# Performance work log

Hardware: AMD Instinct MI355X
Metric: run time of the kernel (lower is better)

The kernel has to match this reference:

```python
import jax, jax.numpy as jnp
import numpy as np

NUM_HEADS = 8
WIN = (7, 7)


def _relative_position_index(wh, ww):
    # Same construction as the torch module (numpy, static).
    coords = np.stack(np.meshgrid(np.arange(wh), np.arange(ww), indexing='ij'))  # (2, wh, ww)
    flat = coords.reshape(2, -1)                                                 # (2, L)
    rel = flat[:, :, None] - flat[:, None, :]                                    # (2, L, L)
    rel = rel.transpose(1, 2, 0).astype(np.int64)                                # (L, L, 2)
    rel[:, :, 0] += wh - 1
    rel[:, :, 1] += ww - 1
    rel[:, :, 0] *= 2 * ww - 1
    return rel.sum(-1)  # (L, L), values in [0, (2wh-1)*(2ww-1))


def setup_inputs() -> dict:
    key = jax.random.key(0)
    k0, k1, k2, k3, k4 = jax.random.split(key, 5)
    B, C = 2048, 256
    wh, ww = WIN
    L = wh * ww
    nW = 64
    q = jax.random.normal(k0, (B, C, wh, ww), dtype=jnp.float32)
    k = jax.random.normal(k1, (B, C, wh, ww), dtype=jnp.float32)
    v = jax.random.normal(k2, (B, C, wh, ww), dtype=jnp.float32)
    # Swin-style shift mask: 0 where attend, -100 where blocked
    keep = jax.random.uniform(k3, (nW, L, L)) < 0.9
    mask = jnp.where(keep, 0.0, -100.0).astype(jnp.float32)
    n_bias = (2 * wh - 1) * (2 * ww - 1)  # 169
    rel_bias_table = 0.02 * jax.random.normal(k4, (n_bias, NUM_HEADS), dtype=jnp.float32)
    rel_pos_index = jnp.asarray(_relative_position_index(wh, ww), dtype=jnp.int32)
    return {"q": q, "k": k, "v": v, "mask": mask,
            "rel_bias_table": rel_bias_table, "rel_pos_index": rel_pos_index}


def reference(q, k, v, mask, rel_bias_table, rel_pos_index):
    b, c, wh, ww = q.shape
    L = wh * ww
    H = NUM_HEADS
    d_k = c // H
    scale = d_k ** -0.5
    qh = q.reshape(b, H, d_k, L)
    kh = k.reshape(b, H, d_k, L)
    # NOTE: the original torch code reassigns v = k.reshape(...) — values come from k.
    vh = kh
    attn = jnp.einsum('bhct,bhcs->bhts', qh, kh) * scale  # (b, H, L, L)
    bias = rel_bias_table[rel_pos_index.reshape(-1)].reshape(L, L, H)
    attn = attn + jnp.transpose(bias, (2, 0, 1))[None]    # (1, H, L, L)
    nW = mask.shape[0]
    attn = attn.reshape(b // nW, nW, H, L, L) + mask[None, :, None]
    attn = attn.reshape(b, H, L, L)
    attn = jax.nn.softmax(attn, axis=-1)
    score = jnp.einsum('bhts,bhcs->bhct', attn, vh).reshape(b, c, wh, ww)
    return (score, attn)
```

## Files before the change

kernel.cpp:

```cpp
#include <hip/hip_runtime.h>
#include <hip/hip_bf16.h>
#include <math.h>


#define LW 49
#define NH 8

typedef short s16x8 __attribute__((ext_vector_type(8)));
typedef float f32x4 __attribute__((ext_vector_type(4)));
typedef unsigned short u16x4 __attribute__((ext_vector_type(4)));

union Frag { s16x8 v; unsigned short u[8]; };

__device__ __forceinline__ unsigned short f2bf(float x) {
    return __builtin_bit_cast(unsigned short, __float2bfloat16(x));
}
__device__ __forceinline__ float bf2f(unsigned short h) {
    return __uint_as_float(((unsigned)h) << 16);
}
__device__ __forceinline__ void split8(const float* xf, Frag& hi, Frag& lo) {
    #pragma unroll
    for (int j = 0; j < 8; j++) {
        const unsigned short hb = f2bf(xf[j]);
        hi.u[j] = hb;
        lo.u[j] = f2bf(xf[j] - bf2f(hb));
    }
}

__device__ __forceinline__ void lds_barrier() {
    asm volatile("s_waitcnt lgkmcnt(0)" ::: "memory");
    __builtin_amdgcn_s_barrier();
    asm volatile("" ::: "memory");
    __builtin_amdgcn_sched_barrier(0);
}

#define MFMA16(A, B, C) __builtin_amdgcn_mfma_f32_16x16x32_bf16((A), (B), (C), 0, 0, 0)

__global__ __launch_bounds__(256) void prep_frag_kernel(
    const float* __restrict__ mask, const float* __restrict__ table,
    const int* __restrict__ idx,
    unsigned short* __restrict__ biasB, unsigned short* __restrict__ maskB)
{
    const int i = blockIdx.x * 256 + threadIdx.x;
    const int NBF = 8 * 4096;
    const int NMF = 64 * 4096;
    const float L2E = 1.4426950408889634f;
    if (i < NBF) {
        const int h = i >> 12, rem = i & 4095;
        const int gi = rem >> 8, lane = (rem >> 2) & 63, r = rem & 3;
        const int mt = gi >> 2, nt = gi & 3;
        const int t = mt * 16 + (lane >> 4) * 4 + r;
        const int s = nt * 16 + (lane & 15);
        const float v = (t < LW && s < LW)
                      ? table[idx[t * LW + s] * NH + h] * L2E : 0.f;
        biasB[i] = f2bf(v);
    } else if (i < NBF + NMF) {
        const int j = i - NBF;
        const int w2 = j >> 12, rem = j & 4095;
        const int gi = rem >> 8, lane = (rem >> 2) & 63, r = rem & 3;
        const int mt = gi >> 2, nt = gi & 3;
        const int t = mt * 16 + (lane >> 4) * 4 + r;
        const int s = nt * 16 + (lane & 15);
        const float v = (t < LW && s < LW)
                      ? mask[w2 * (LW * LW) + t * LW + s] * L2E : 0.f;
        maskB[j] = f2bf(v);
    }
}

__global__ __launch_bounds__(128, 4) void wa_mfma_kernel(
    const float* __restrict__ q, const float* __restrict__ k,
    const unsigned short* __restrict__ biasB,
    const unsigned short* __restrict__ maskB,
    float* __restrict__ score_out, float* __restrict__ attn_out)
{
    __shared__ __align__(16) unsigned short sB[6272];

    const int wv   = __builtin_amdgcn_readfirstlane((int)(threadIdx.x >> 6));
    const int bh   = blockIdx.x;
    const int h    = bh & 7;
    const int w    = (bh >> 3) & 63;
    const int lane = threadIdx.x & 63;
    const int l15  = lane & 15;
    const int g4   = lane >> 4;

    const float* qp = q + (size_t)bh * (32 * LW);
    const float* kp = k + (size_t)bh * (32 * LW);

    float k1raw[2][8], qraw[2][8], k2raw[2][8];
    #pragma unroll
    for (int ki = 0; ki < 2; ki++) {
        const int s  = (wv * 2 + ki) * 16 + l15;
        const int sc = s < LW ? s : (LW - 1);
        #pragma unroll
        for (int j = 0; j < 8; j++) k1raw[ki][j] = kp[(g4 * 8 + j) * LW + sc];
    }
    #pragma unroll
    for (int mi = 0; mi < 2; mi++) {
        const int t  = (wv * 2 + mi) * 16 + l15;
        const int tc = t < LW ? t : (LW - 1);
        #pragma unroll
        for (int j = 0; j < 8; j++) qraw[mi][j] = qp[(g4 * 8 + j) * LW + tc];
    }
    {
        const int c = wv * 16 + l15;
        #pragma unroll
        for (int ks = 0; ks < 2; ks++)
            #pragma unroll
            for (int j = 0; j < 8; j++) {
                const int s  = ks * 32 + g4 * 8 + j;
                const int sc = s < LW ? s : (LW - 1);
                k2raw[ks][j] = kp[c * LW + sc];
            }
    }

    u16x4 bq4[2][4], mq4[2][4];
    {
        const unsigned short* bF = biasB + (size_t)h * 4096 + lane * 4;
        const unsigned short* mF = maskB + (size_t)w * 4096 + lane * 4;
        #pragma unroll
        for (int mi = 0; mi < 2; mi++)
            #pragma unroll
            for (int nt = 0; nt < 4; nt++) {
                const int gi = (wv * 2 + mi) * 4 + nt;
                bq4[mi][nt] = *(const u16x4*)(bF + gi * 256);
                mq4[mi][nt] = *(const u16x4*)(mF + gi * 256);
            }
    }

    #pragma unroll
    for (int ki = 0; ki < 2; ki++) {
        const int nt = wv * 2 + ki;
        Frag Kh, Kl;
        split8(k1raw[ki], Kh, Kl);
        *(s16x8*)&sB[nt * 512 + lane * 8]        = Kh.v;
        *(s16x8*)&sB[2048 + nt * 512 + lane * 8] = Kl.v;
    }

    Frag Qh[2], Ql[2];
    split8(qraw[0], Qh[0], Ql[0]);
    split8(qraw[1], Qh[1], Ql[1]);

    lds_barrier();

    f32x4 acc[2][4];
    #pragma unroll
    for (int mi = 0; mi < 2; mi++)
        #pragma unroll
        for (int nt = 0; nt < 4; nt++)
            #pragma unroll
            for (int r = 0; r < 4; r++) acc[mi][nt][r] = 0.f;

    #pragma unroll
    for (int nt = 0; nt < 4; nt++) {
        Frag Kh, Kl;
        Kh.v = *(const s16x8*)&sB[nt * 512 + lane * 8];
        Kl.v = *(const s16x8*)&sB[2048 + nt * 512 + lane * 8];
        #pragma unroll
        for (int mi = 0; mi < 2; mi++) {
            acc[mi][nt] = MFMA16(Qh[mi].v, Kh.v, acc[mi][nt]);
            acc[mi][nt] = MFMA16(Ql[mi].v, Kh.v, acc[mi][nt]);
            acc[mi][nt] = MFMA16(Qh[mi].v, Kl.v, acc[mi][nt]);
        }
    }

    const float scale2 = 0.17677669529663687f * 1.4426950408889634f;
    #pragma unroll
    for (int mi = 0; mi < 2; mi++) {
        #pragma unroll
        for (int nt = 0; nt < 4; nt++) {
            const bool pad = (nt * 16 + l15) >= LW;
            #pragma unroll
            for (int r = 0; r < 4; r++) {
                const float bm = bf2f(bq4[mi][nt][r]) + bf2f(mq4[mi][nt][r]);
                const float v2 = fmaf(acc[mi][nt][r], scale2, bm);
                acc[mi][nt][r] = pad ? -1e30f : v2;
            }
        }
    }

    #pragma unroll
    for (int mi = 0; mi < 2; mi++) {
        #pragma unroll
        for (int r = 0; r < 4; r++) {
            float sm = 0.f;
            #pragma unroll
            for (int nt = 0; nt < 4; nt++) {
                const float p = __builtin_exp2f(acc[mi][nt][r]);
                acc[mi][nt][r] = p;
                sm += p;
            }
            sm += __shfl_xor(sm, 1);
            sm += __shfl_xor(sm, 2);
            sm += __shfl_xor(sm, 4);
            sm += __shfl_xor(sm, 8);
            const float inv = 1.0f / sm;
            #pragma unroll
            for (int nt = 0; nt < 4; nt++) acc[mi][nt][r] *= inv;
        }
    }

    lds_barrier();

    #pragma unroll
    for (int mi = 0; mi < 2; mi++) {
        #pragma unroll
        for (int r = 0; r < 4; r++) {
            const int t = (wv * 2 + mi) * 16 + g4 * 4 + r;
            if (t < LW) {
                #pragma unroll
                for (int nt = 0; nt < 4; nt++) {
                    const int s = nt * 16 + l15;
                    const float p = acc[mi][nt][r];
                    const unsigned short ph = f2bf(p);
                    const unsigned short pl = f2bf(p - bf2f(ph));
                    const unsigned idx = (unsigned)t * 64u
                        + ((((unsigned)s >> 3) ^ ((unsigned)t & 7u)) << 3)
                        + ((unsigned)s & 7u);
                    sB[idx]        = ph;
                    sB[3136 + idx] = pl;
                }
            }
        }
    }

    lds_barrier();

    float* attn_base = attn_out + (size_t)bh * (LW * LW);
    #pragma unroll
    for (int mi = 0; mi < 2; mi++) {
        #pragma unroll
        for (int r = 0; r < 4; r++) {
            const int t = (wv * 2 + mi) * 16 + g4 * 4 + r;
            if (t < LW) {
                #pragma unroll
                for (int nt = 0; nt < 4; nt++) {
                    const int s = nt * 16 + l15;
                    if (s < LW) attn_base[t * LW + s] = acc[mi][nt][r];
                }
            }
        }
    }

    Frag K2h[2], K2l[2];
    split8(k2raw[0], K2h[0], K2l[0]);
    split8(k2raw[1], K2h[1], K2l[1]);

    f32x4 acc2[4];
    #pragma unroll
    for (int nt = 0; nt < 4; nt++)
        #pragma unroll
        for (int r = 0; r < 4; r++) acc2[nt][r] = 0.f;

    #pragma unroll
    for (int ntt = 0; ntt < 4; ntt++) {
        const int t  = ntt * 16 + l15;
        const int tr = t < LW ? t : (LW - 1);
        #pragma unroll
        for (int ks = 0; ks < 2; ks++) {
            const unsigned base = (unsigned)tr * 64u
                + (((unsigned)(ks * 4 + g4) ^ ((unsigned)tr & 7u)) << 3);
            Frag Ph, Pl;
            Ph.v = *(const s16x8*)&sB[base];
            Pl.v = *(const s16x8*)&sB[3136 + base];
            acc2[ntt] = MFMA16(K2h[ks].v, Ph.v, acc2[ntt]);
            acc2[ntt] = MFMA16(K2l[ks].v, Ph.v, acc2[ntt]);
            acc2[ntt] = MFMA16(K2h[ks].v, Pl.v, acc2[ntt]);
        }
    }

    float* scp = score_out + (size_t)bh * (32 * LW);
    #pragma unroll
    for (int ntt = 0; ntt < 4; ntt++) {
        const int t = ntt * 16 + l15;
        if (t < LW) {
            #pragma unroll
            for (int r = 0; r < 4; r++) {
                const int c = wv * 16 + g4 * 4 + r;
                scp[c * LW + t] = acc2[ntt][r];
            }
        }
    }
}

__global__ __launch_bounds__(256, 4) void wa_fallback_kernel(
    const float* __restrict__ q, const float* __restrict__ k,
    const float* __restrict__ mask0, const float* __restrict__ table,
    const int* __restrict__ idx,
    float* __restrict__ score_out, float* __restrict__ attn_out)
{
    __shared__ float sPf[LW * LW];
    const int lane = threadIdx.x & 63;
    const int wv   = __builtin_amdgcn_readfirstlane((int)(threadIdx.x >> 6));
    const int bh   = blockIdx.x * 4 + wv;
    const int h    = bh & 7;
    const int w    = (bh >> 3) & 63;
    const int t    = lane;
    const int tc   = (t < LW) ? t : (LW - 1);

    const float* qp = q + (size_t)bh * (32 * LW);
    const float* kp = k + (size_t)bh * (32 * LW);

    float qreg[32];
    #pragma unroll
    for (int c = 0; c < 32; c++) qreg[c] = qp[c * LW + tc];

    float S[LW];
    #pragma unroll
    for (int s = 0; s < LW; s++) S[s] = 0.f;
    #pragma unroll
    for (int c = 0; c < 32; c++) {
        #pragma unroll
        for (int s = 0; s < LW; s++)
            S[s] = fmaf(qreg[c], kp[c * LW + s], S[s]);
    }

    const float scale = 0.17677669529663687f;
    const float* mrow = mask0 + (size_t)w * (LW * LW) + tc * LW;
    const int*   irow = idx + tc * LW;
    #pragma unroll
    for (int s = 0; s < LW; s++) {
        const float bm = table[irow[s] * NH + h] + mrow[s];
        S[s] = fmaf(S[s], scale, bm);
    }

    float m = S[0];
    #pragma unroll
    for (int s = 1; s < LW; s++) m = fmaxf(m, S[s]);
    float sum = 0.f;
    #pragma unroll
    for (int s = 0; s < LW; s++) { S[s] = __expf(S[s] - m); sum += S[s]; }
    const float invs = 1.0f / sum;
    #pragma unroll
    for (int s = 0; s < LW; s++) S[s] *= invs;

    float* attn_base = attn_out + (size_t)bh * (LW * LW);
    for (int turn = 0; turn < 4; turn++) {
        __syncthreads();
        if (turn == wv) {
            if (t < LW) {
                #pragma unroll
                for (int s = 0; s < LW; s++) sPf[t * LW + s] = S[s];
            }
            #pragma unroll
            for (int it = 0; it < 38; it++) {
                const int i = it * 64 + lane;
                if (i < LW * LW) attn_base[i] = sPf[i];
            }
        }
    }

    float* sc = score_out + (size_t)bh * (32 * LW);
    #pragma unroll
    for (int c = 0; c < 32; c++) {
        float a = 0.f;
        #pragma unroll
        for (int s = 0; s < LW; s++) a = fmaf(S[s], kp[c * LW + s], a);
        if (t < LW) sc[c * LW + t] = a;
    }
}

extern "C" void kernel_launch(void* const* d_in, const int* in_sizes, int n_in,
                              void* d_out, int out_size, void* d_ws, size_t ws_size,
                              hipStream_t stream) {
    const float* q     = (const float*)d_in[0];
    const float* k     = (const float*)d_in[1];
    const float* mask  = (const float*)d_in[3];
    const float* table = (const float*)d_in[4];
    const int*   idx   = (const int*)d_in[5];

    float* score_out = (float*)d_out;
    float* attn_out  = score_out + (size_t)2048 * 256 * 49;

    const size_t NBF = (size_t)8 * 4096;
    const size_t NMF = (size_t)64 * 4096;

    if (ws_size >= (NBF + NMF) * sizeof(unsigned short)) {
        unsigned short* biasB = (unsigned short*)d_ws;
        unsigned short* maskB = biasB + NBF;
        const int tot = (int)(NBF + NMF);
        prep_frag_kernel<<<(tot + 255) / 256, 256, 0, stream>>>(
            mask, table, idx, biasB, maskB);
        wa_mfma_kernel<<<16384, 128, 0, stream>>>(
            q, k, biasB, maskB, score_out, attn_out);
    } else {
        wa_fallback_kernel<<<4096, 256, 0, stream>>>(
            q, k, mask, table, idx, score_out, attn_out);
    }
}
```

Measured before the change: 497.3 us.

## Stage Q and K tiles into LDS via direct global-to-LDS loads

Replaces the strided per-thread global gathers of Q and K with contiguous 16-byte global_load_lds copies. Wave 0 copies K and wave 1 copies Q into a shared buffer, followed by one barrier. All fragments (Q, K for QK^T, and K for PV) are then read from LDS and each lane splits its own K fragments, instead of round-tripping split K through LDS. The aim is coalesced global traffic and less redundant reading of the same K data. In exchange the kernel needs more shared memory, a full vmcnt wait before compute, and some strided LDS reads that may hit bank conflicts.

```diff
diff --git a/kernel.cpp b/kernel.cpp
--- a/kernel.cpp
+++ b/kernel.cpp
@@ -32,6 +32,18 @@
     __builtin_amdgcn_s_barrier();
     asm volatile("" ::: "memory");
     __builtin_amdgcn_sched_barrier(0);
+}
+__device__ __forceinline__ void stage_barrier() {
+    asm volatile("s_waitcnt vmcnt(0) lgkmcnt(0)" ::: "memory");
+    __builtin_amdgcn_s_barrier();
+    asm volatile("" ::: "memory");
+    __builtin_amdgcn_sched_barrier(0);
+}
+
+__device__ __forceinline__ void load_lds16(const void* g, void* l) {
+    __builtin_amdgcn_global_load_lds(
+        (const __attribute__((address_space(1))) void*)g,
+        (__attribute__((address_space(3))) void*)l, 16, 0, 0);
 }
 
 #define MFMA16(A, B, C) __builtin_amdgcn_mfma_f32_16x16x32_bf16((A), (B), (C), 0, 0, 0)
@@ -73,7 +85,7 @@
     const unsigned short* __restrict__ maskB,
     float* __restrict__ score_out, float* __restrict__ attn_out)
 {
-    __shared__ __align__(16) unsigned short sB[6272];
+    __shared__ __align__(16) char sRaw[12800];
 
     const int wv   = __builtin_amdgcn_readfirstlane((int)(threadIdx.x >> 6));
     const int bh   = blockIdx.x;
@@ -86,32 +98,22 @@
     const float* qp = q + (size_t)bh * (32 * LW);
     const float* kp = k + (size_t)bh * (32 * LW);
 
-    float k1raw[2][8], qraw[2][8], k2raw[2][8];
-    #pragma unroll
-    for (int ki = 0; ki < 2; ki++) {
-        const int s  = (wv * 2 + ki) * 16 + l15;
-        const int sc = s < LW ? s : (LW - 1);
-        #pragma unroll
-        for (int j = 0; j < 8; j++) k1raw[ki][j] = kp[(g4 * 8 + j) * LW + sc];
-    }
-    #pragma unroll
-    for (int mi = 0; mi < 2; mi++) {
-        const int t  = (wv * 2 + mi) * 16 + l15;
-        const int tc = t < LW ? t : (LW - 1);
-        #pragma unroll
-        for (int j = 0; j < 8; j++) qraw[mi][j] = qp[(g4 * 8 + j) * LW + tc];
-    }
+    char* ldsK = sRaw;
+    char* ldsQ = sRaw + 6400;
+
     {
-        const int c = wv * 16 + l15;
-        #pragma unroll
-        for (int ks = 0; ks < 2; ks++)
-            #pragma unroll
-            for (int j = 0; j < 8; j++) {
-                const int s  = ks * 32 + g4 * 8 + j;
-                const int sc = s < LW ? s : (LW - 1);
-                k2raw[ks][j] = kp[c * LW + sc];
-            }
-    }
+        const char* src = (wv == 0) ? (const char*)kp : (const char*)qp;
+        char*       dst = (wv == 0) ? ldsK : ldsQ;
+        #pragma unroll
+        for (int i = 0; i < 6; i++)
+            load_lds16(src + i * 1024 + lane * 16, dst + i * 1024);
+        if (lane < 16) {
+            const int off = (lane < 8) ? lane * 16 : 112;
+            load_lds16(src + 6144 + off, dst + 6144);
+        }
+    }
+
+    stage_barrier();
 
     u16x4 bq4[2][4], mq4[2][4];
     {
@@ -127,39 +129,58 @@
             }
     }
 
-    #pragma unroll
-    for (int ki = 0; ki < 2; ki++) {
-        const int nt = wv * 2 + ki;
+    const float* sKf = (const float*)ldsK;
+    const float* sQf = (const float*)ldsQ;
+
+    Frag Qh[2], Ql[2];
+    #pragma unroll
+    for (int mi = 0; mi < 2; mi++) {
+        const int t  = (wv * 2 + mi) * 16 + l15;
+        const int tc = t < LW ? t : (LW - 1);
+        float xf[8];
+        #pragma unroll
+        for (int j = 0; j < 8; j++) xf[j] = sQf[(g4 * 8 + j) * LW + tc];
+        split8(xf, Qh[mi], Ql[mi]);
+    }
+
+    f32x4 acc[2][4];
+    #pragma unroll
+    for (int mi = 0; mi < 2; mi++)
+        #pragma unroll
+        for (int nt = 0; nt < 4; nt++)
+            #pragma unroll
+            for (int r = 0; r < 4; r++) acc[mi][nt][r] = 0.f;
+
+    #pragma unroll
+    for (int nt = 0; nt < 4; nt++) {
+        const int s  = nt * 16 + l15;
+        const int sc = s < LW ? s : (LW - 1);
+        float xf[8];
+        #pragma unroll
+        for (int j = 0; j < 8; j++) xf[j] = sKf[(g4 * 8 + j) * LW + sc];
         Frag Kh, Kl;
-        split8(k1raw[ki], Kh, Kl);
-        *(s16x8*)&sB[nt * 512 + lane * 8]        = Kh.v;
-        *(s16x8*)&sB[2048 + nt * 512 + lane * 8] = Kl.v;
-    }
-
-    Frag Qh[2], Ql[2];
-    split8(qraw[0], Qh[0], Ql[0]);
-    split8(qraw[1], Qh[1], Ql[1]);
-
-    lds_barrier();
-
-    f32x4 acc[2][4];
-    #pragma unroll
-    for (int mi = 0; mi < 2; mi++)
-        #pragma unroll
-        for (int nt = 0; nt < 4; nt++)
-            #pragma unroll
-            for (int r = 0; r < 4; r++) acc[mi][nt][r] = 0.f;
-
-    #pragma unroll
-    for (int nt = 0; nt < 4; nt++) {
-        Frag Kh, Kl;
-        Kh.v = *(const s16x8*)&sB[nt * 512 + lane * 8];
-        Kl.v = *(const s16x8*)&sB[2048 + nt * 512 + lane * 8];
+        split8(xf, Kh, Kl);
         #pragma unroll
         for (int mi = 0; mi < 2; mi++) {
             acc[mi][nt] = MFMA16(Qh[mi].v, Kh.v, acc[mi][nt]);
             acc[mi][nt] = MFMA16(Ql[mi].v, Kh.v, acc[mi][nt]);
             acc[mi][nt] = MFMA16(Qh[mi].v, Kl.v, acc[mi][nt]);
+        }
+    }
+
+    Frag K2h[2], K2l[2];
+    {
+        const int c = wv * 16 + l15;
+        #pragma unroll
+        for (int ks = 0; ks < 2; ks++) {
+            float xf[8];
+            #pragma unroll
+            for (int j = 0; j < 8; j++) {
+                const int s  = ks * 32 + g4 * 8 + j;
+                const int sc = s < LW ? s : (LW - 1);
+                xf[j] = sKf[c * LW + sc];
+            }
+            split8(xf, K2h[ks], K2l[ks]);
         }
     }
 
@@ -201,6 +222,7 @@
 
     lds_barrier();
 
+    unsigned short* sB = (unsigned short*)sRaw;
     #pragma unroll
     for (int mi = 0; mi < 2; mi++) {
         #pragma unroll
@@ -241,10 +263,6 @@
         }
     }
 
-    Frag K2h[2], K2l[2];
-    split8(k2raw[0], K2h[0], K2l[0]);
-    split8(k2raw[1], K2h[1], K2l[1]);
-
     f32x4 acc2[4];
     #pragma unroll
     for (int nt = 0; nt < 4; nt++)
```

New measurement: 461.1 us. 1.08x faster.
